# Kernel tuning notes

Hardware: AMD Instinct MI355X
Metric: run time of the kernel (lower is better)

Reference implementation:

```python
import jax, jax.numpy as jnp
import numpy as np

EPSILON = 1e-8
MASK_INDEX = 1023  # == num_categories - 1

B, L, N = 16, 4096, 1024


def setup_inputs() -> dict:
    key = jax.random.key(0)
    k1, k2, k3, k4 = jax.random.split(key, 4)
    x = jax.random.randint(k1, (B, L), 0, MASK_INDEX)          # data tokens, never the mask token
    u = jax.random.uniform(k2, (1,), dtype=jnp.float32)         # shared time offset (torch.rand(1))
    noise = jax.random.uniform(k3, (B, L), dtype=jnp.float32)   # per-position masking noise
    W = jax.random.normal(k4, (N, N), dtype=jnp.float32) * 0.02 # denoiser weight: one_hot(z) @ W
    return {"x": x, "u": u, "noise": noise, "W": W}


def reference(x, u, noise, W):
    b, l = x.shape
    n = W.shape[0]
    # t_i = (u + i/B) mod 1 ; linear masking schedule: alpha(t)=1-t, alpha'(t)=-1
    t = jnp.remainder(u + jnp.arange(b, dtype=jnp.float32) / b, 1.0)  # [B]
    alpha = 1.0 - t
    # weight = alpha'(t) / clamp(1 - alpha, eps) = -1 / clamp(t, eps)
    weight = -1.0 / jnp.maximum(1.0 - alpha, EPSILON)
    # Categorical(alpha*one_hot(x) + (1-alpha)*one_hot(mask)) == Bernoulli remask:
    # keep original token w.p. alpha, else mask token. O(B*L) instead of O(B*L*N).
    keep = noise < alpha[:, None]                                  # [B, L] bool
    z_t = jnp.where(keep, x, MASK_INDEX)                            # [B, L] int
    # denoiser: x_theta = softmax(one_hot(z_t) @ W)  (one-hot matmul == row gather)
    logits = W[z_t]                                                 # [B, L, N]
    logp = jax.nn.log_softmax(logits, axis=-1)                      # [B, L, N]
    # log((x_theta * one_hot(x)).sum(-1)) == log_softmax gathered at x
    loss_terms = jnp.take_along_axis(logp, x[..., None], axis=-1)[..., 0]  # [B, L]
    loss = weight * loss_terms.sum(axis=-1)                         # [B]
    return loss.mean(axis=0)                                        # scalar
```

## Files before the change

kernel.cpp:

```cpp
#include <hip/hip_runtime.h>

#define N_CAT    1024
#define B_DIM    16
#define L_DIM    4096
#define MASK_IDX 1023
#define EPS      1e-8f

__global__ __launch_bounds__(256) void lse_kernel(const float* __restrict__ W,
                                                  float* __restrict__ lse,
                                                  float* __restrict__ D) {
    const int r   = blockIdx.x;
    const int tid = threadIdx.x;

    const float4 v = *reinterpret_cast<const float4*>(W + (size_t)r * N_CAT + tid * 4);

    float m = fmaxf(fmaxf(v.x, v.y), fmaxf(v.z, v.w));
    #pragma unroll
    for (int off = 32; off > 0; off >>= 1)
        m = fmaxf(m, __shfl_down(m, off, 64));

    __shared__ float smax[4];
    __shared__ float ssum[4];
    const int wave = tid >> 6, lane = tid & 63;
    if (lane == 0) smax[wave] = m;
    __syncthreads();
    const float bm = fmaxf(fmaxf(smax[0], smax[1]), fmaxf(smax[2], smax[3]));

    float s = expf(v.x - bm) + expf(v.y - bm) + expf(v.z - bm) + expf(v.w - bm);
    #pragma unroll
    for (int off = 32; off > 0; off >>= 1)
        s += __shfl_down(s, off, 64);
    if (lane == 0) ssum[wave] = s;
    __syncthreads();

    if (tid == 0) {
        const float l = bm + logf(ssum[0] + ssum[1] + ssum[2] + ssum[3]);
        lse[r] = l;
        D[r]   = W[(size_t)r * N_CAT + r] - l;
    }
}

__global__ __launch_bounds__(256) void loss_kernel(const int*   __restrict__ x,
                                                   const float* __restrict__ u,
                                                   const float* __restrict__ noise,
                                                   const float* __restrict__ W,
                                                   const float* __restrict__ lse,
                                                   const float* __restrict__ D,
                                                   float* __restrict__ out) {
    const int b   = blockIdx.x >> 2;
    const int seg = blockIdx.x & 3;
    const int tid = threadIdx.x;

    const float t     = fmodf(u[0] + (float)b * (1.0f / (float)B_DIM), 1.0f);
    const float alpha = 1.0f - t;
    const float wgt   = -1.0f / fmaxf(t, EPS);
    const float lseM  = lse[MASK_IDX];
    const float* WmaskRow = W + (size_t)MASK_IDX * N_CAT;

    const int base = b * L_DIM + seg * 1024 + tid * 4;
    const int4   xv = *reinterpret_cast<const int4*>(x + base);
    const float4 nv = *reinterpret_cast<const float4*>(noise + base);

    const int   xs[4] = {xv.x, xv.y, xv.z, xv.w};
    const float ns[4] = {nv.x, nv.y, nv.z, nv.w};

    float sum = 0.0f;
    #pragma unroll
    for (int i = 0; i < 4; ++i) {
        const int xi = xs[i];
        const float term = (ns[i] < alpha) ? D[xi] : (WmaskRow[xi] - lseM);
        sum += term;
    }

    #pragma unroll
    for (int off = 32; off > 0; off >>= 1)
        sum += __shfl_down(sum, off, 64);

    __shared__ float swave[4];
    const int wave = tid >> 6, lane = tid & 63;
    if (lane == 0) swave[wave] = sum;
    __syncthreads();

    if (wave == 0) {
        float v = (lane < 4) ? swave[lane] : 0.0f;
        #pragma unroll
        for (int off = 2; off > 0; off >>= 1)
            v += __shfl_down(v, off, 64);
        if (lane == 0)
            atomicAdd(out, wgt * v * (1.0f / (float)B_DIM));
    }
}

extern "C" void kernel_launch(void* const* d_in, const int* in_sizes, int n_in,
                              void* d_out, int out_size, void* d_ws, size_t ws_size,
                              hipStream_t stream) {
    const int*   x     = (const int*)  d_in[0];
    const float* u     = (const float*)d_in[1];
    const float* noise = (const float*)d_in[2];
    const float* W     = (const float*)d_in[3];
    float*       out   = (float*)d_out;

    float* lse = (float*)d_ws;
    float* D   = (float*)d_ws + N_CAT;

    hipMemsetAsync(out, 0, sizeof(float), stream);

    lse_kernel<<<N_CAT, 256, 0, stream>>>(W, lse, D);
    loss_kernel<<<B_DIM * 4, 256, 0, stream>>>(x, u, noise, W, lse, D, out);
}
```

Before: 68.03 us.

## Fold output zeroing into lse kernel and spread loss over one thread per token

Drops the separate memset launch by having the first thread of the lse kernel zero the output. The loss kernel now processes one token per thread across 256 blocks instead of four tokens per thread across 64 blocks, which raises parallelism for the gather-heavy work. Each thread applies its batch weight before the reduction. The cost is four times as many atomics on a single address and scalar rather than vector loads.

Result: no change. 67.68 us (-0.5%).

```diff
diff --git a/kernel.cpp b/kernel.cpp
--- a/kernel.cpp
+++ b/kernel.cpp
@@ -8,9 +8,12 @@
 
 __global__ __launch_bounds__(256) void lse_kernel(const float* __restrict__ W,
                                                   float* __restrict__ lse,
-                                                  float* __restrict__ D) {
+                                                  float* __restrict__ D,
+                                                  float* __restrict__ out) {
     const int r   = blockIdx.x;
     const int tid = threadIdx.x;
+
+    if (r == 0 && tid == 0) out[0] = 0.0f;
 
     const float4 v = *reinterpret_cast<const float4*>(W + (size_t)r * N_CAT + tid * 4);
 
@@ -47,30 +50,21 @@
                                                    const float* __restrict__ lse,
                                                    const float* __restrict__ D,
                                                    float* __restrict__ out) {
-    const int b   = blockIdx.x >> 2;
-    const int seg = blockIdx.x & 3;
+    const int gid = blockIdx.x * 256 + threadIdx.x;
+    const int b   = gid >> 12;
     const int tid = threadIdx.x;
 
     const float t     = fmodf(u[0] + (float)b * (1.0f / (float)B_DIM), 1.0f);
     const float alpha = 1.0f - t;
     const float wgt   = -1.0f / fmaxf(t, EPS);
     const float lseM  = lse[MASK_IDX];
-    const float* WmaskRow = W + (size_t)MASK_IDX * N_CAT;
+    const float* __restrict__ WmaskRow = W + (size_t)MASK_IDX * N_CAT;
 
-    const int base = b * L_DIM + seg * 1024 + tid * 4;
-    const int4   xv = *reinterpret_cast<const int4*>(x + base);
-    const float4 nv = *reinterpret_cast<const float4*>(noise + base);
+    const int   xi = x[gid];
+    const float ni = noise[gid];
 
-    const int   xs[4] = {xv.x, xv.y, xv.z, xv.w};
-    const float ns[4] = {nv.x, nv.y, nv.z, nv.w};
-
-    float sum = 0.0f;
-    #pragma unroll
-    for (int i = 0; i < 4; ++i) {
-        const int xi = xs[i];
-        const float term = (ns[i] < alpha) ? D[xi] : (WmaskRow[xi] - lseM);
-        sum += term;
-    }
+    const float term = (ni < alpha) ? D[xi] : (WmaskRow[xi] - lseM);
+    float sum = wgt * term * (1.0f / (float)B_DIM);
 
     #pragma unroll
     for (int off = 32; off > 0; off >>= 1)
@@ -87,7 +81,7 @@
         for (int off = 2; off > 0; off >>= 1)
             v += __shfl_down(v, off, 64);
         if (lane == 0)
-            atomicAdd(out, wgt * v * (1.0f / (float)B_DIM));
+            atomicAdd(out, v);
     }
 }
 
@@ -103,8 +97,6 @@
     float* lse = (float*)d_ws;
     float* D   = (float*)d_ws + N_CAT;
 
-    hipMemsetAsync(out, 0, sizeof(float), stream);
-
-    lse_kernel<<<N_CAT, 256, 0, stream>>>(W, lse, D);
-    loss_kernel<<<B_DIM * 4, 256, 0, stream>>>(x, u, noise, W, lse, D, out);
+    lse_kernel<<<N_CAT, 256, 0, stream>>>(W, lse, D, out);
+    loss_kernel<<<(B_DIM * L_DIM) / 256, 256, 0, stream>>>(x, u, noise, W, lse, D, out);
 }
```
